# Kernel tuning notes

Hardware: AMD Instinct MI355X
Metric: run time of the kernel (lower is better)

The kernel has to match this reference:

```python
import jax, jax.numpy as jnp
import numpy as np

D_MODEL = 1024
NUM_HEADS = 16
HEAD_DIM = D_MODEL // NUM_HEADS
SCALE = HEAD_DIM ** -0.5


def setup_inputs() -> dict:
    key = jax.random.key(0)
    k1, k2, k3 = jax.random.split(key, 3)
    x = jax.random.normal(k1, (4, 2048, D_MODEL), dtype=jnp.float32)
    # torch Linear stores weight [out, in]; we store transposed [in, out] for x @ W
    w_qkv = jax.random.normal(k2, (D_MODEL, 3 * D_MODEL), dtype=jnp.float32) * (D_MODEL ** -0.5)
    w_out = jax.random.normal(k3, (D_MODEL, D_MODEL), dtype=jnp.float32) * (D_MODEL ** -0.5)
    return {"x": x, "w_qkv": w_qkv, "w_out": w_out}


def reference(x, w_qkv, w_out):
    batch, seq_len, _ = x.shape
    qkv = x @ w_qkv  # [B, S, 3*D]
    q, k, v = jnp.split(qkv, 3, axis=-1)

    def to_heads(t):
        return t.reshape(batch, seq_len, NUM_HEADS, HEAD_DIM).transpose(0, 2, 1, 3)  # [B, H, S, Dh]

    q, k, v = to_heads(q), to_heads(k), to_heads(v)
    attn = jnp.einsum('bhqd,bhkd->bhqk', q, k) * SCALE  # [B, H, S, S]
    causal = jnp.tril(jnp.ones((seq_len, seq_len), dtype=bool))
    attn = jnp.where(causal[None, None], attn, -jnp.inf)
    attn = jax.nn.softmax(attn, axis=-1)
    out = jnp.einsum('bhqk,bhkd->bhqd', attn, v)  # [B, H, S, Dh]
    out = out.transpose(0, 2, 1, 3).reshape(batch, seq_len, D_MODEL)
    return out @ w_out
```

## Files before the change

kernel.cpp:

```cpp
#include <hip/hip_runtime.h>
#include <hip/hip_bf16.h>

typedef unsigned short u16;
typedef float f32x4 __attribute__((ext_vector_type(4)));
typedef __bf16 bf16x8 __attribute__((ext_vector_type(8)));
typedef u16 u16x8 __attribute__((ext_vector_type(8)));
typedef u16 u16x4 __attribute__((ext_vector_type(4)));
typedef unsigned u32x2 __attribute__((ext_vector_type(2)));

__device__ __forceinline__ u16 f2bf(float f) {
  unsigned u = __builtin_bit_cast(unsigned, f);
  u = (u + 0x7fffu + ((u >> 16) & 1u)) >> 16;
  return (u16)u;
}

__device__ __forceinline__ unsigned cvtpk(float lo, float hi) {
  unsigned r;
  asm("v_cvt_pk_bf16_f32 %0, %1, %2" : "=v"(r) : "v"(lo), "v"(hi));
  return r;
}

__device__ __forceinline__ float exp2b(float x) {
  return __builtin_amdgcn_exp2f(x);
}

__device__ __forceinline__ void gload16(const void* g, void* l) {
  __builtin_amdgcn_global_load_lds(
      (const __attribute__((address_space(1))) unsigned*)g,
      (__attribute__((address_space(3))) unsigned*)l, 16, 0, 0);
}

__device__ __forceinline__ f32x4 mfma16(bf16x8 a, bf16x8 b, f32x4 c) {
  return __builtin_amdgcn_mfma_f32_16x16x32_bf16(a, b, c, 0, 0, 0);
}

__global__ __launch_bounds__(256) void convx(const float4* __restrict__ x,
                                             u16x8* __restrict__ xb, int n) {
  int i = blockIdx.x * 256 + threadIdx.x;
  if (i >= n) return;
  float4 a = x[2 * i], b = x[2 * i + 1];
  u16x8 o;
  o[0] = f2bf(a.x); o[1] = f2bf(a.y); o[2] = f2bf(a.z); o[3] = f2bf(a.w);
  o[4] = f2bf(b.x); o[5] = f2bf(b.y); o[6] = f2bf(b.z); o[7] = f2bf(b.w);
  xb[i] = o;
}

__global__ __launch_bounds__(256) void transpose_w(const float* __restrict__ w,
                                                   u16* __restrict__ wt,
                                                   int R, int C) {
  __shared__ float tile[32][33];
  int n0 = blockIdx.x * 32, k0 = blockIdx.y * 32;
  int tx = threadIdx.x & 31, ty = threadIdx.x >> 5;
#pragma unroll
  for (int j = 0; j < 32; j += 8)
    tile[ty + j][tx] = w[(size_t)(k0 + ty + j) * C + n0 + tx];
  __syncthreads();
#pragma unroll
  for (int j = 0; j < 32; j += 8)
    wt[(size_t)(n0 + ty + j) * R + k0 + tx] = f2bf(tile[tx][ty + j]);
}

template <int MODE, int BM, int BN, int WGM, int WGN>
__global__ __launch_bounds__(512, 2) void gemm_t(const u16* __restrict__ A,
                                                 const u16* __restrict__ Bt,
                                                 void* __restrict__ Cv,
                                                 int M, int N, int K,
                                                 u16* __restrict__ Qb,
                                                 u16* __restrict__ Kb) {
  constexpr int PWM = BM / WGM, PWN = BN / WGN;
  constexpr int MI = PWM / 16;
  static_assert(PWN == 64, "per-wave N must be 64 (NI=4)");
  constexpr int ALD = BM / 128, BLD = BN / 128, LPT = ALD + BLD;
  __shared__ alignas(16) u16 As[4][BM][32];
  __shared__ alignas(16) u16 Bs[4][BN][32];
  const int tix = threadIdx.x;
  const int lane = tix & 63, wid = tix >> 6;
  const int wm = wid / WGN, wn = wid % WGN;
  const int r = lane & 15, g = lane >> 4;
  const int s2 = (r >> 1) & 3;
  const int m0 = blockIdx.y * BM, n0 = blockIdx.x * BN;

  const int srow = tix >> 2;
  const int swc = (tix & 3) ^ ((srow >> 1) & 3);
  const u16* gA[ALD];
  const u16* gB[BLD];
#pragma unroll
  for (int i = 0; i < ALD; ++i)
    gA[i] = A + (size_t)(m0 + i * 128 + srow) * K + swc * 8;
#pragma unroll
  for (int i = 0; i < BLD; ++i)
    gB[i] = Bt + (size_t)(n0 + i * 128 + srow) * K + swc * 8;

  auto SA = [&](int tt) {
    const int ko = tt * 32, bu_ = tt & 3;
#pragma unroll
    for (int i = 0; i < ALD; ++i)
      gload16(gA[i] + ko, &As[bu_][i * 128 + wid * 16][0]);
  };
  auto SB = [&](int tt) {
    const int ko = tt * 32, bu_ = tt & 3;
#pragma unroll
    for (int i = 0; i < BLD; ++i)
      gload16(gB[i] + ko, &Bs[bu_][i * 128 + wid * 16][0]);
  };

  f32x4 acc[MI][4] = {};
  const int NT = K >> 5;

  SA(0); SB(0); SA(1); SB(1); SA(2); SB(2);

  for (int t = 0; t < NT; ++t) {
    if (t < NT - 2) {
      if constexpr (LPT == 4) asm volatile("s_waitcnt vmcnt(8)" ::: "memory");
      else                    asm volatile("s_waitcnt vmcnt(6)" ::: "memory");
    } else if (t == NT - 2) {
      if constexpr (LPT == 4) asm volatile("s_waitcnt vmcnt(4)" ::: "memory");
      else                    asm volatile("s_waitcnt vmcnt(3)" ::: "memory");
    } else {
      asm volatile("s_waitcnt vmcnt(0)" ::: "memory");
    }
    __builtin_amdgcn_s_barrier();
    __builtin_amdgcn_sched_barrier(0);

    const int bu = t & 3;
    if (t + 3 < NT) SA(t + 3);
    bf16x8 af[MI];
#pragma unroll
    for (int mi = 0; mi < MI; ++mi)
      af[mi] = *(const bf16x8*)&As[bu][wm * PWM + mi * 16 + r][(g ^ s2) * 8];
    bf16x8 b0 = *(const bf16x8*)&Bs[bu][wn * 64 + r][(g ^ s2) * 8];
    bf16x8 b1 = *(const bf16x8*)&Bs[bu][wn * 64 + 16 + r][(g ^ s2) * 8];
#pragma unroll
    for (int mi = 0; mi < MI; ++mi) acc[mi][0] = mfma16(af[mi], b0, acc[mi][0]);
#pragma unroll
    for (int mi = 0; mi < MI; ++mi) acc[mi][1] = mfma16(af[mi], b1, acc[mi][1]);
    if (t + 3 < NT) SB(t + 3);
    bf16x8 b2 = *(const bf16x8*)&Bs[bu][wn * 64 + 32 + r][(g ^ s2) * 8];
    bf16x8 b3 = *(const bf16x8*)&Bs[bu][wn * 64 + 48 + r][(g ^ s2) * 8];
#pragma unroll
    for (int mi = 0; mi < MI; ++mi) acc[mi][2] = mfma16(af[mi], b2, acc[mi][2]);
#pragma unroll
    for (int mi = 0; mi < MI; ++mi) acc[mi][3] = mfma16(af[mi], b3, acc[mi][3]);
  }

#pragma unroll
  for (int mi = 0; mi < MI; ++mi) {
    int row = m0 + wm * PWM + mi * 16 + g * 4;
#pragma unroll
    for (int ni = 0; ni < 4; ++ni) {
      int col = n0 + wn * 64 + ni * 16 + r;
#pragma unroll
      for (int e = 0; e < 4; ++e) {
        float v = acc[mi][ni][e];
        int rr = row + e;
        if (MODE == 0) {
          ((u16*)Cv)[(size_t)rr * N + col] = f2bf(v);
        } else if (MODE == 2) {
          ((float*)Cv)[(size_t)rr * N + col] = v;
        } else {
          int which = col >> 10, hh = (col >> 6) & 15, dd = col & 63;
          int bb = rr >> 11, ss = rr & 2047;
          size_t idx = ((size_t)(bb * 16 + hh) * 2048 + ss) * 64 + dd;
          (which ? Kb : Qb)[idx] = f2bf(which ? v : v * 0.18033688011112042f);
        }
      }
    }
  }
}

__global__ __launch_bounds__(512, 6) void attn_fwd(const u16* __restrict__ Q,
                                                   const u16* __restrict__ Kc,
                                                   const u16* __restrict__ Vt,
                                                   u16* __restrict__ O) {
  __shared__ alignas(16) u16 Ks[2][64][64];
  __shared__ alignas(16) u16 Vs[2][64][64];
  __shared__ alignas(16) u16 Ps[8][16][72];
  const int lane = threadIdx.x & 63, wid = threadIdx.x >> 6;
  const int r = lane & 15, g = lane >> 4;
  const int bh = blockIdx.x, b = bh >> 4, h = bh & 15;
  const int qb = 15 - (int)blockIdx.y;
  const int qw = qb * 128 + wid * 16;
  const int nkv = 2 * (qb + 1);

  const u16* Kp = Kc + (size_t)bh * 2048 * 64;
  const u16* Vp = Vt + (size_t)(h * 64) * 8192 + (size_t)b * 2048;
  const u16* Qp = Q + ((size_t)bh * 2048 + qw) * 64;
  u16* pw = &Ps[wid][0][0];

  const int srow = lane >> 3;
  const int scol = ((lane & 7) ^ srow) * 8;

  bf16x8 qf[2];
  qf[0] = *(const bf16x8*)(Qp + (size_t)r * 64 + g * 8);
  qf[1] = *(const bf16x8*)(Qp + (size_t)r * 64 + 32 + g * 8);

  u16x8 ov8;
#pragma unroll
  for (int i = 0; i < 8; ++i) ov8[i] = 0x3F80;
  const bf16x8 ones = __builtin_bit_cast(bf16x8, ov8);

  f32x4 o[5] = {};

  gload16(Kp + (size_t)(wid * 8 + srow) * 64 + scol, &Ks[0][wid * 8][0]);
  gload16(Vp + (size_t)(wid * 8 + srow) * 8192 + scol, &Vs[0][wid * 8][0]);

  int cur = 0;
  for (int t = 0; t < nkv; ++t, cur ^= 1) {
    __syncthreads();
    if (t + 1 < nkv) {
      const int kn = (t + 1) * 64;
      gload16(Kp + (size_t)(kn + wid * 8 + srow) * 64 + scol, &Ks[cur ^ 1][wid * 8][0]);
      gload16(Vp + (size_t)(wid * 8 + srow) * 8192 + kn + scol, &Vs[cur ^ 1][wid * 8][0]);
    }
    const int kv0 = t * 64;
    if (kv0 > qw + 15) continue;

    f32x4 s[4];
    __builtin_amdgcn_s_setprio(1);
#pragma unroll
    for (int tt = 0; tt < 4; ++tt) {
      bf16x8 k0 = *(const bf16x8*)&Ks[cur][tt * 16 + r][((0 + g) ^ (r & 7)) * 8];
      bf16x8 k1 = *(const bf16x8*)&Ks[cur][tt * 16 + r][((4 + g) ^ (r & 7)) * 8];
      f32x4 z = {-16.f, -16.f, -16.f, -16.f};
      z = mfma16(k0, qf[0], z);
      z = mfma16(k1, qf[1], z);
      s[tt] = z;
    }
    __builtin_amdgcn_s_setprio(0);
    if (kv0 + 63 > qw) {
#pragma unroll
      for (int tt = 0; tt < 4; ++tt) {
        int kvb = kv0 + tt * 16 + g * 4;
#pragma unroll
        for (int e = 0; e < 4; ++e)
          if (kvb + e > qw + r) s[tt][e] = -1e30f;
      }
    }

#pragma unroll
    for (int tt = 0; tt < 4; ++tt) {
      float p0 = exp2b(s[tt][0]), p1 = exp2b(s[tt][1]);
      float p2 = exp2b(s[tt][2]), p3 = exp2b(s[tt][3]);
      u32x2 w;
      w[0] = cvtpk(p0, p1);
      w[1] = cvtpk(p2, p3);
      *(u32x2*)&pw[r * 72 + tt * 16 + g * 4] = w;
    }

    bf16x8 pB0 = *(const bf16x8*)&pw[r * 72 + g * 8];
    bf16x8 pB1 = *(const bf16x8*)&pw[r * 72 + 32 + g * 8];
    __builtin_amdgcn_s_setprio(1);
#pragma unroll
    for (int dt = 0; dt < 4; ++dt) {
      bf16x8 v0 = *(const bf16x8*)&Vs[cur][dt * 16 + r][((0 + g) ^ (r & 7)) * 8];
      bf16x8 v1 = *(const bf16x8*)&Vs[cur][dt * 16 + r][((4 + g) ^ (r & 7)) * 8];
      o[dt] = mfma16(v0, pB0, o[dt]);
      o[dt] = mfma16(v1, pB1, o[dt]);
    }
    o[4] = mfma16(ones, pB0, o[4]);
    o[4] = mfma16(ones, pB1, o[4]);
    __builtin_amdgcn_s_setprio(0);
  }

  float inv = 1.f / o[4][0];
  size_t rowbase = ((size_t)b * 2048 + qw + r) * 1024 + h * 64;
#pragma unroll
  for (int dt = 0; dt < 4; ++dt) {
    u16x4 ov;
#pragma unroll
    for (int e = 0; e < 4; ++e) ov[e] = f2bf(o[dt][e] * inv);
    *(u16x4*)&O[rowbase + dt * 16 + g * 4] = ov;
  }
}

extern "C" void kernel_launch(void* const* d_in, const int* in_sizes, int n_in,
                              void* d_out, int out_size, void* d_ws,
                              size_t ws_size, hipStream_t stream) {
  const float* x = (const float*)d_in[0];
  const float* wqkv = (const float*)d_in[1];
  const float* wout = (const float*)d_in[2];
  float* out = (float*)d_out;
  char* ws = (char*)d_ws;

  u16* Xb = (u16*)ws;
  u16* Wt = (u16*)(ws + (16ull << 20));
  u16* WoT = (u16*)(ws + (22ull << 20));
  u16* Qb = (u16*)(ws + (24ull << 20));
  u16* Kb = (u16*)(ws + (40ull << 20));
  u16* Vt = (u16*)(ws + (56ull << 20));

  convx<<<4096, 256, 0, stream>>>((const float4*)x, (u16x8*)Xb, 1048576);
  transpose_w<<<dim3(96, 32), 256, 0, stream>>>(wqkv, Wt, 1024, 3072);
  transpose_w<<<dim3(32, 32), 256, 0, stream>>>(wout, WoT, 1024, 1024);

  gemm_t<1, 256, 256, 2, 4><<<dim3(8, 32), 512, 0, stream>>>(
      Xb, Wt, nullptr, 8192, 2048, 1024, Qb, Kb);
  gemm_t<0, 128, 256, 2, 4><<<dim3(32, 8), 512, 0, stream>>>(
      Wt + (size_t)2048 * 1024, Xb, Vt, 1024, 8192, 1024, nullptr, nullptr);
  attn_fwd<<<dim3(64, 16), 512, 0, stream>>>(Qb, Kb, Vt, Xb);
  gemm_t<2, 256, 128, 4, 2><<<dim3(8, 32), 512, 0, stream>>>(
      Xb, WoT, out, 8192, 1024, 1024, nullptr, nullptr);
}
```

Before: 184.1 us.

## Split GEMM main loop into two M-halves with barriers and MFMA priority boosts

Restructures the GEMM inner loop so all four B fragments are loaded once up front and the M dimension is processed in two halves, each an LDS-load phase followed by an MFMA cluster. Extra workgroup barriers, explicit lgkmcnt waits and s_setprio raises around the MFMA clusters are added to keep waves in lockstep and interleave memory and compute phases across waves. This adds two barriers per K-step, which may cost more than the better overlap gains, and changes register pressure under the 2-block launch bound.

```diff
diff --git a/kernel.cpp b/kernel.cpp
--- a/kernel.cpp
+++ b/kernel.cpp
@@ -68,7 +68,7 @@
                                                  u16* __restrict__ Qb,
                                                  u16* __restrict__ Kb) {
   constexpr int PWM = BM / WGM, PWN = BN / WGN;
-  constexpr int MI = PWM / 16;
+  constexpr int MI = PWM / 16, MH = MI / 2;
   static_assert(PWN == 64, "per-wave N must be 64 (NI=4)");
   constexpr int ALD = BM / 128, BLD = BN / 128, LPT = ALD + BLD;
   __shared__ alignas(16) u16 As[4][BM][32];
@@ -123,24 +123,41 @@
     __builtin_amdgcn_sched_barrier(0);
 
     const int bu = t & 3;
+    bf16x8 a0[MH], bf[4];
+#pragma unroll
+    for (int mi = 0; mi < MH; ++mi)
+      a0[mi] = *(const bf16x8*)&As[bu][wm * PWM + mi * 16 + r][(g ^ s2) * 8];
+#pragma unroll
+    for (int ni = 0; ni < 4; ++ni)
+      bf[ni] = *(const bf16x8*)&Bs[bu][wn * 64 + ni * 16 + r][(g ^ s2) * 8];
     if (t + 3 < NT) SA(t + 3);
-    bf16x8 af[MI];
-#pragma unroll
-    for (int mi = 0; mi < MI; ++mi)
-      af[mi] = *(const bf16x8*)&As[bu][wm * PWM + mi * 16 + r][(g ^ s2) * 8];
-    bf16x8 b0 = *(const bf16x8*)&Bs[bu][wn * 64 + r][(g ^ s2) * 8];
-    bf16x8 b1 = *(const bf16x8*)&Bs[bu][wn * 64 + 16 + r][(g ^ s2) * 8];
-#pragma unroll
-    for (int mi = 0; mi < MI; ++mi) acc[mi][0] = mfma16(af[mi], b0, acc[mi][0]);
-#pragma unroll
-    for (int mi = 0; mi < MI; ++mi) acc[mi][1] = mfma16(af[mi], b1, acc[mi][1]);
+    __builtin_amdgcn_s_barrier();
+    asm volatile("s_waitcnt lgkmcnt(0)" ::: "memory");
+    __builtin_amdgcn_sched_barrier(0);
+    __builtin_amdgcn_s_setprio(1);
+#pragma unroll
+    for (int mi = 0; mi < MH; ++mi)
+#pragma unroll
+      for (int ni = 0; ni < 4; ++ni)
+        acc[mi][ni] = mfma16(a0[mi], bf[ni], acc[mi][ni]);
+    __builtin_amdgcn_s_setprio(0);
+    __builtin_amdgcn_s_barrier();
+
+    bf16x8 a1[MH];
+#pragma unroll
+    for (int mi = 0; mi < MH; ++mi)
+      a1[mi] = *(const bf16x8*)&As[bu][wm * PWM + (MH + mi) * 16 + r][(g ^ s2) * 8];
     if (t + 3 < NT) SB(t + 3);
-    bf16x8 b2 = *(const bf16x8*)&Bs[bu][wn * 64 + 32 + r][(g ^ s2) * 8];
-    bf16x8 b3 = *(const bf16x8*)&Bs[bu][wn * 64 + 48 + r][(g ^ s2) * 8];
-#pragma unroll
-    for (int mi = 0; mi < MI; ++mi) acc[mi][2] = mfma16(af[mi], b2, acc[mi][2]);
-#pragma unroll
-    for (int mi = 0; mi < MI; ++mi) acc[mi][3] = mfma16(af[mi], b3, acc[mi][3]);
+    __builtin_amdgcn_s_barrier();
+    asm volatile("s_waitcnt lgkmcnt(0)" ::: "memory");
+    __builtin_amdgcn_sched_barrier(0);
+    __builtin_amdgcn_s_setprio(1);
+#pragma unroll
+    for (int mi = 0; mi < MH; ++mi)
+#pragma unroll
+      for (int ni = 0; ni < 4; ++ni)
+        acc[MH + mi][ni] = mfma16(a1[mi], bf[ni], acc[MH + mi][ni]);
+    __builtin_amdgcn_s_setprio(0);
   }
 
 #pragma unroll
```

New measurement: 168.2 us. -8.6%, faster.
